# Kernel optimization log

Measured on AMD Instinct MI355X. Metric: run time of the kernel, lower is better.

The kernel has to match this reference:

```python
import jax, jax.numpy as jnp
import numpy as np

NUM_BLOCKS_PER_ROW = 64
NUM_BLOCKS_PER_COLUMN = 36
N = NUM_BLOCKS_PER_ROW * NUM_BLOCKS_PER_COLUMN  # 2304 nodes per frame
F = 32   # frames in the GOP (linear reference chain)
B = 1024  # batch = number of candidate anchor points
S = 256   # selected anchor points


def setup_inputs() -> dict:
    key = jax.random.key(0)
    k1, k2, k3, k4 = jax.random.split(key, 4)
    # weights[f] propagates cumulated error from frame f -> frame f+1; scaled small
    # so the 31-step propagation chain stays numerically tame.
    weights = jax.random.normal(k1, (F - 1, N, N), dtype=jnp.float32) * 0.02
    biases = jax.random.uniform(k2, (F, N), dtype=jnp.float32)  # per-frame tc bias
    selected_anchor_points = jax.random.randint(k3, (S, 3), 0, 32, dtype=jnp.int32)
    candidate_anchor_points = jax.random.randint(k4, (B, 3), 0, 32, dtype=jnp.int32)
    return {
        "weights": weights,
        "biases": biases,
        "selected_anchor_points": selected_anchor_points,
        "candidate_anchor_points": candidate_anchor_points,
    }


def _forward(weights, biases, selected_anchor_points, candidate_anchor_points):
    dtype = biases.dtype
    # flatten (row, col) -> node index, same as row * num_blocks_per_row + col
    sel_f = selected_anchor_points[:, 0]
    sel_node = selected_anchor_points[:, 1] * NUM_BLOCKS_PER_ROW + selected_anchor_points[:, 2]
    cand_f = candidate_anchor_points[:, 0]
    cand_node = candidate_anchor_points[:, 1] * NUM_BLOCKS_PER_ROW + candidate_anchor_points[:, 2]

    # selected anchors zero a node's column for ALL batch rows in their frame
    keep_sel = jnp.ones((F, N), dtype=dtype).at[sel_f, sel_node].set(0.0)  # [F, N]
    # candidate anchors zero one (batch, node) entry in their frame
    cand_oh = jax.nn.one_hot(cand_node, N, dtype=dtype)  # [B, N]

    def apply_masks(err, f):
        # err: [B, N] cumulated error of frame f
        err = err * keep_sel[f][None, :]
        kill = (cand_f == f).astype(dtype)[:, None] * cand_oh  # [B, N]
        return err * (1.0 - kill)

    # root (key) frame: bias only
    err0 = apply_masks(jnp.broadcast_to(biases[0], (B, N)), 0)
    total0 = jnp.sum(err0, axis=1)  # [B]

    def step(carry, xs):
        prev_err, total = carry
        w_f, b_f, f = xs
        # torch.sparse.mm(W, prev.T).T == prev @ W.T
        cur = b_f[None, :] + jnp.matmul(prev_err, w_f.T)  # [B, N]
        cur = apply_masks(cur, f)
        return (cur, total + jnp.sum(cur, axis=1)), None

    frame_ids = jnp.arange(1, F)
    (_, total), _ = jax.lax.scan(step, (err0, total0), (weights, biases[1:], frame_ids))
    return total  # [B] per-candidate summed error


def reference(weights, biases, selected_anchor_points, candidate_anchor_points):
    return _forward(weights, biases, selected_anchor_points, candidate_anchor_points)
```

## Files before the change

kernel.cpp:

```cpp
#include <hip/hip_runtime.h>
#include <stdint.h>

#define NN 2304
#define NF 32
#define NB 1024
#define NS 256

#define BM 128
#define BN 96
#define BK 64
#define KSLICES (NN / BK)
#define DEPTH 4
#define NGRP 8
#define GRPBLKS 24

typedef short bf16x8 __attribute__((ext_vector_type(8)));
typedef float f32x4  __attribute__((ext_vector_type(4)));

__device__ __forceinline__ unsigned short f2bf(float f) {
  union { float f; unsigned u; } v; v.f = f;
  return (unsigned short)((v.u + 0x7FFFu + ((v.u >> 16) & 1u)) >> 16);
}

__device__ __forceinline__ void async16(const void* g, void* l) {
  __builtin_amdgcn_global_load_lds((const __attribute__((address_space(1))) void*)g,
                                   (__attribute__((address_space(3))) void*)l, 16, 0, 0);
}

#define WAITV(n) asm volatile("s_waitcnt vmcnt(" #n ")" ::: "memory")

__global__ void init_kernel(const f32x4* __restrict__ W4, const int* __restrict__ sel,
                            const int* __restrict__ cand, bf16x8* __restrict__ Wb8,
                            float* __restrict__ keep, int* __restrict__ cf,
                            int* __restrict__ cn, float* __restrict__ out,
                            int* __restrict__ bar) {
  int gid = blockIdx.x * 256 + threadIdx.x;
  if (gid < (31 * NN * NN) / 8) {
    f32x4 x = W4[2 * gid], y = W4[2 * gid + 1];
    bf16x8 o;
    o[0] = (short)f2bf(x[0]); o[1] = (short)f2bf(x[1]);
    o[2] = (short)f2bf(x[2]); o[3] = (short)f2bf(x[3]);
    o[4] = (short)f2bf(y[0]); o[5] = (short)f2bf(y[1]);
    o[6] = (short)f2bf(y[2]); o[7] = (short)f2bf(y[3]);
    Wb8[gid] = o;
  }
  if (gid < NF * NN) {
    int f = gid / NN, n = gid - f * NN;
    float v = 1.0f;
    for (int s = 0; s < NS; ++s) {
      int sf = sel[3 * s], sn = sel[3 * s + 1] * 64 + sel[3 * s + 2];
      if (sf == f && sn == n) v = 0.0f;
    }
    keep[gid] = v;
  }
  if (gid < NB) {
    cf[gid] = cand[3 * gid];
    cn[gid] = cand[3 * gid + 1] * 64 + cand[3 * gid + 2];
    out[gid] = 0.f;
  }
  if (gid < NGRP * NF) bar[gid] = 0;
}

__device__ __forceinline__ void group_barrier(int* cnt, int t) {
  __syncthreads();
  if (t == 0) {
    __builtin_amdgcn_fence(__ATOMIC_RELEASE, "agent");
    __hip_atomic_fetch_add(cnt, 1, __ATOMIC_RELAXED, __HIP_MEMORY_SCOPE_AGENT);
    while (__hip_atomic_load(cnt, __ATOMIC_RELAXED, __HIP_MEMORY_SCOPE_AGENT) < GRPBLKS)
      __builtin_amdgcn_s_sleep(2);
    __builtin_amdgcn_fence(__ATOMIC_ACQUIRE, "agent");
  }
  __syncthreads();
}

__launch_bounds__(512, 2)
__global__ void persist_kernel(const unsigned short* __restrict__ Wb,
                               const float* __restrict__ biases,
                               const float* __restrict__ keep,
                               const int* __restrict__ cf, const int* __restrict__ cn,
                               unsigned short* __restrict__ errA,
                               unsigned short* __restrict__ errB,
                               float* __restrict__ out, int* __restrict__ bar) {
  __shared__ __align__(16) unsigned char sA[DEPTH][BM * BK * 2];
  __shared__ __align__(16) unsigned char sB[DEPTH][BN * BK * 2];

  const int t = threadIdx.x;
  const int l = t & 63, w = t >> 6;
  const int wm = w >> 1, wn = w & 1;
  const int id = blockIdx.x;
  const int g = id & 7;
  const int mBase = g * BM;
  const int nBase = (id >> 3) * BN;

  {
    const int row = mBase + (t >> 2);
    const int c0 = nBase + (t & 3) * 24;
    const int kn = (cf[row] == 0) ? cn[row] : -1;
    float sum = 0.f;
    for (int j = 0; j < 24; ++j) {
      const int col = c0 + j;
      float v = biases[col] * keep[col];
      if (col == kn) v = 0.f;
      errA[row * NN + col] = f2bf(v);
      sum += v;
    }
    sum += __shfl_xor(sum, 1, 64);
    sum += __shfl_xor(sum, 2, 64);
    if ((t & 3) == 0) atomicAdd(&out[row], sum);
  }
  group_barrier(&bar[g * NF + 0], t);

  const int sRow = l >> 3;
  const int sCk = (l & 7) ^ sRow;
  const bool aRole = (w < 4);
  const int rw = aRole ? w : (w - 4);
  const int ldsOff = aRole ? (rw * 32 * 128 + l * 16) : (rw * 24 * 128 + l * 16);
  const int gRowOff = aRole ? ((mBase + rw * 32 + sRow) * NN + sCk * 8)
                            : ((nBase + rw * 24 + sRow) * NN + sCk * 8);

  const int fl = l & 15, q = l >> 4;
  const int fragB0 = (q ^ (fl & 7)) * 16;

  for (int f = 1; f < NF; ++f) {
    const unsigned short* Ain = (f & 1) ? errA : errB;
    unsigned short* errOut = (f & 1) ? errB : errA;
    const unsigned short* gSrc =
        (aRole ? Ain : Wb + (size_t)(f - 1) * NN * NN) + gRowOff;
    const float* biasf = biases + f * NN;
    const float* keepf = keep + f * NN;

    f32x4 acc[2][3];
#pragma unroll
    for (int r = 0; r < 2; ++r)
#pragma unroll
      for (int c = 0; c < 3; ++c) acc[r][c] = (f32x4){0.f, 0.f, 0.f, 0.f};

#pragma unroll
    for (int p = 0; p < DEPTH; ++p) {
      const unsigned short* gp = gSrc + p * BK;
      if (aRole) {
        unsigned char* la = &sA[p][ldsOff];
#pragma unroll
        for (int c = 0; c < 4; ++c) async16(gp + c * 8 * NN, la + c * 8 * 128);
      } else {
        unsigned char* lb = &sB[p][ldsOff];
#pragma unroll
        for (int c = 0; c < 3; ++c) async16(gp + c * 8 * NN, lb + c * 8 * 128);
      }
    }

    int buf = 0;
    for (int s = 0; s < KSLICES; ++s) {
      const int ahead = KSLICES - 1 - s;
      if (ahead >= 3) { if (aRole) WAITV(12); else WAITV(9); }
      else if (ahead == 2) { if (aRole) WAITV(8); else WAITV(6); }
      else if (ahead == 1) { if (aRole) WAITV(4); else WAITV(3); }
      else { WAITV(0); }
      asm volatile("s_barrier" ::: "memory");

      const unsigned char* pa = &sA[buf][(wm * 32 + fl) * 128];
      const unsigned char* pb = &sB[buf][(wn * 48 + fl) * 128];
#pragma unroll
      for (int h = 0; h < 2; ++h) {
        const int cb = fragB0 ^ (h * 64);
        bf16x8 aF[2], bF[3];
#pragma unroll
        for (int r = 0; r < 2; ++r) aF[r] = *(const bf16x8*)(pa + r * 2048 + cb);
#pragma unroll
        for (int c = 0; c < 3; ++c) bF[c] = *(const bf16x8*)(pb + c * 2048 + cb);
#pragma unroll
        for (int r = 0; r < 2; ++r)
#pragma unroll
          for (int c = 0; c < 3; ++c)
            acc[r][c] = __builtin_amdgcn_mfma_f32_16x16x32_bf16(aF[r], bF[c], acc[r][c], 0, 0, 0);
      }
      asm volatile("s_waitcnt lgkmcnt(0)\n\ts_barrier" ::: "memory");
      if (s + DEPTH < KSLICES) {
        const unsigned short* gp = gSrc + (s + DEPTH) * BK;
        if (aRole) {
          unsigned char* la = &sA[buf][ldsOff];
#pragma unroll
          for (int c = 0; c < 4; ++c) async16(gp + c * 8 * NN, la + c * 8 * 128);
        } else {
          unsigned char* lb = &sB[buf][ldsOff];
#pragma unroll
          for (int c = 0; c < 3; ++c) async16(gp + c * 8 * NN, lb + c * 8 * 128);
        }
      }
      buf = (buf == DEPTH - 1) ? 0 : buf + 1;
    }

#pragma unroll
    for (int r = 0; r < 2; ++r) {
      float rs[4] = {0.f, 0.f, 0.f, 0.f};
      const int rowB = mBase + wm * 32 + r * 16 + q * 4;
#pragma unroll
      for (int c = 0; c < 3; ++c) {
        const int col = nBase + wn * 48 + c * 16 + fl;
        const float kv = keepf[col], bv = biasf[col];
#pragma unroll
        for (int i = 0; i < 4; ++i) {
          const int row = rowB + i;
          float v = (acc[r][c][i] + bv) * kv;
          if (cf[row] == f && cn[row] == col) v = 0.f;
          errOut[row * NN + col] = f2bf(v);
          rs[i] += v;
        }
      }
#pragma unroll
      for (int m = 1; m < 16; m <<= 1) {
#pragma unroll
        for (int i = 0; i < 4; ++i) rs[i] += __shfl_xor(rs[i], m, 64);
      }
      if (fl == 0) {
#pragma unroll
        for (int i = 0; i < 4; ++i) atomicAdd(&out[rowB + i], rs[i]);
      }
    }

    group_barrier(&bar[g * NF + f], t);
  }
}

extern "C" void kernel_launch(void* const* d_in, const int* in_sizes, int n_in,
                              void* d_out, int out_size, void* d_ws, size_t ws_size,
                              hipStream_t stream) {
  (void)in_sizes; (void)n_in; (void)out_size; (void)ws_size;
  const float* W = (const float*)d_in[0];
  const float* biases = (const float*)d_in[1];
  const int* sel = (const int*)d_in[2];
  const int* cand = (const int*)d_in[3];
  float* out = (float*)d_out;
  char* ws = (char*)d_ws;

  size_t off = 0;
  unsigned short* Wb = (unsigned short*)(ws + off); off += (size_t)31 * NN * NN * 2;
  float* keep = (float*)(ws + off); off += (size_t)NF * NN * 4;
  int* cf = (int*)(ws + off); off += NB * 4;
  int* cn = (int*)(ws + off); off += NB * 4;
  int* bar = (int*)(ws + off); off += NGRP * NF * 4;
  off = (off + 255) & ~(size_t)255;
  unsigned short* errA = (unsigned short*)(ws + off); off += (size_t)NB * NN * 2;
  unsigned short* errB = (unsigned short*)(ws + off);

  int convBlocks = (31 * NN * NN / 8 + 255) / 256;
  init_kernel<<<convBlocks, 256, 0, stream>>>((const f32x4*)W, sel, cand, (bf16x8*)Wb,
                                              keep, cf, cn, out, bar);

  const unsigned short* WbC = Wb;
  void* kargs[] = {(void*)&WbC, (void*)&biases, (void*)&keep, (void*)&cf, (void*)&cn,
                   (void*)&errA, (void*)&errB, (void*)&out, (void*)&bar};
  hipError_t e = hipLaunchCooperativeKernel(
      reinterpret_cast<void*>(persist_kernel), dim3(NGRP * GRPBLKS), dim3(512),
      kargs, 0, stream);
  if (e != hipSuccess) {
    persist_kernel<<<NGRP * GRPBLKS, 512, 0, stream>>>(Wb, biases, keep, cf, cn,
                                                       errA, errB, out, bar);
  }
}
```

Baseline: 1.969 ms.

## Split init kernel, scatter selected masks, and use five-buffer LDS ring

The monolithic init kernel is split into a grid-stride weight conversion, a mask build that fills keep with ones, and a small scatter kernel that zeroes the selected-anchor entries. This replaces the per-element 256-iteration loop over selected anchors. The GEMM main loop now uses five LDS buffers with separate read and write indices, so the next slice's async load is issued right after the barrier. That removes the second barrier and the lgkmcnt wait per slice, and s_setprio raises priority around the MFMA block. The extra buffer increases LDS use per block, which could limit occupancy under the 2-blocks-per-CU launch bound.

```diff
diff --git a/kernel.cpp b/kernel.cpp
--- a/kernel.cpp
+++ b/kernel.cpp
@@ -11,6 +11,7 @@
 #define BK 64
 #define KSLICES (NN / BK)
 #define DEPTH 4
+#define NBUF 5
 #define NGRP 8
 #define GRPBLKS 24
 
@@ -29,13 +30,9 @@
 
 #define WAITV(n) asm volatile("s_waitcnt vmcnt(" #n ")" ::: "memory")
 
-__global__ void init_kernel(const f32x4* __restrict__ W4, const int* __restrict__ sel,
-                            const int* __restrict__ cand, bf16x8* __restrict__ Wb8,
-                            float* __restrict__ keep, int* __restrict__ cf,
-                            int* __restrict__ cn, float* __restrict__ out,
-                            int* __restrict__ bar) {
-  int gid = blockIdx.x * 256 + threadIdx.x;
-  if (gid < (31 * NN * NN) / 8) {
+__global__ void convert_w(const f32x4* __restrict__ W4, bf16x8* __restrict__ Wb8) {
+  const int total = (31 * NN * NN) / 8;
+  for (int gid = blockIdx.x * 256 + threadIdx.x; gid < total; gid += gridDim.x * 256) {
     f32x4 x = W4[2 * gid], y = W4[2 * gid + 1];
     bf16x8 o;
     o[0] = (short)f2bf(x[0]); o[1] = (short)f2bf(x[1]);
@@ -44,21 +41,25 @@
     o[6] = (short)f2bf(y[2]); o[7] = (short)f2bf(y[3]);
     Wb8[gid] = o;
   }
-  if (gid < NF * NN) {
-    int f = gid / NN, n = gid - f * NN;
-    float v = 1.0f;
-    for (int s = 0; s < NS; ++s) {
-      int sf = sel[3 * s], sn = sel[3 * s + 1] * 64 + sel[3 * s + 2];
-      if (sf == f && sn == n) v = 0.0f;
-    }
-    keep[gid] = v;
-  }
+}
+
+__global__ void build_masks(const int* __restrict__ cand, float* __restrict__ keep,
+                            int* __restrict__ cf, int* __restrict__ cn,
+                            float* __restrict__ out, int* __restrict__ bar) {
+  int gid = blockIdx.x * 256 + threadIdx.x;
+  if (gid < NF * NN) keep[gid] = 1.0f;
   if (gid < NB) {
     cf[gid] = cand[3 * gid];
     cn[gid] = cand[3 * gid + 1] * 64 + cand[3 * gid + 2];
     out[gid] = 0.f;
   }
   if (gid < NGRP * NF) bar[gid] = 0;
+}
+
+__global__ void scatter_sel(const int* __restrict__ sel, float* __restrict__ keep) {
+  int s = threadIdx.x;
+  int sf = sel[3 * s], sn = sel[3 * s + 1] * 64 + sel[3 * s + 2];
+  keep[sf * NN + sn] = 0.0f;
 }
 
 __device__ __forceinline__ void group_barrier(int* cnt, int t) {
@@ -81,8 +82,8 @@
                                unsigned short* __restrict__ errA,
                                unsigned short* __restrict__ errB,
                                float* __restrict__ out, int* __restrict__ bar) {
-  __shared__ __align__(16) unsigned char sA[DEPTH][BM * BK * 2];
-  __shared__ __align__(16) unsigned char sB[DEPTH][BN * BK * 2];
+  __shared__ __align__(16) unsigned char sA[NBUF][BM * BK * 2];
+  __shared__ __align__(16) unsigned char sB[NBUF][BN * BK * 2];
 
   const int t = threadIdx.x;
   const int l = t & 63, w = t >> 6;
@@ -149,7 +150,7 @@
       }
     }
 
-    int buf = 0;
+    int rbuf = 0, wbuf = DEPTH;
     for (int s = 0; s < KSLICES; ++s) {
       const int ahead = KSLICES - 1 - s;
       if (ahead >= 3) { if (aRole) WAITV(12); else WAITV(9); }
@@ -157,9 +158,22 @@
       else if (ahead == 1) { if (aRole) WAITV(4); else WAITV(3); }
       else { WAITV(0); }
       asm volatile("s_barrier" ::: "memory");
-
-      const unsigned char* pa = &sA[buf][(wm * 32 + fl) * 128];
-      const unsigned char* pb = &sB[buf][(wn * 48 + fl) * 128];
+      if (s + DEPTH < KSLICES) {
+        const unsigned short* gp = gSrc + (s + DEPTH) * BK;
+        if (aRole) {
+          unsigned char* la = &sA[wbuf][ldsOff];
+#pragma unroll
+          for (int c = 0; c < 4; ++c) async16(gp + c * 8 * NN, la + c * 8 * 128);
+        } else {
+          unsigned char* lb = &sB[wbuf][ldsOff];
+#pragma unroll
+          for (int c = 0; c < 3; ++c) async16(gp + c * 8 * NN, lb + c * 8 * 128);
+        }
+      }
+
+      const unsigned char* pa = &sA[rbuf][(wm * 32 + fl) * 128];
+      const unsigned char* pb = &sB[rbuf][(wn * 48 + fl) * 128];
+      __builtin_amdgcn_s_setprio(1);
 #pragma unroll
       for (int h = 0; h < 2; ++h) {
         const int cb = fragB0 ^ (h * 64);
@@ -174,20 +188,9 @@
           for (int c = 0; c < 3; ++c)
             acc[r][c] = __builtin_amdgcn_mfma_f32_16x16x32_bf16(aF[r], bF[c], acc[r][c], 0, 0, 0);
       }
-      asm volatile("s_waitcnt lgkmcnt(0)\n\ts_barrier" ::: "memory");
-      if (s + DEPTH < KSLICES) {
-        const unsigned short* gp = gSrc + (s + DEPTH) * BK;
-        if (aRole) {
-          unsigned char* la = &sA[buf][ldsOff];
-#pragma unroll
-          for (int c = 0; c < 4; ++c) async16(gp + c * 8 * NN, la + c * 8 * 128);
-        } else {
-          unsigned char* lb = &sB[buf][ldsOff];
-#pragma unroll
-          for (int c = 0; c < 3; ++c) async16(gp + c * 8 * NN, lb + c * 8 * 128);
-        }
-      }
-      buf = (buf == DEPTH - 1) ? 0 : buf + 1;
+      __builtin_amdgcn_s_setprio(0);
+      rbuf = (rbuf == NBUF - 1) ? 0 : rbuf + 1;
+      wbuf = (wbuf == NBUF - 1) ? 0 : wbuf + 1;
     }
 
 #pragma unroll
@@ -243,9 +246,9 @@
   unsigned short* errA = (unsigned short*)(ws + off); off += (size_t)NB * NN * 2;
   unsigned short* errB = (unsigned short*)(ws + off);
 
-  int convBlocks = (31 * NN * NN / 8 + 255) / 256;
-  init_kernel<<<convBlocks, 256, 0, stream>>>((const f32x4*)W, sel, cand, (bf16x8*)Wb,
-                                              keep, cf, cn, out, bar);
+  convert_w<<<4096, 256, 0, stream>>>((const f32x4*)W, (bf16x8*)Wb);
+  build_masks<<<(NF * NN + 255) / 256, 256, 0, stream>>>(cand, keep, cf, cn, out, bar);
+  scatter_sel<<<1, NS, 0, stream>>>(sel, keep);
 
   const unsigned short* WbC = Wb;
   void* kargs[] = {(void*)&WbC, (void*)&biases, (void*)&keep, (void*)&cf, (void*)&cn,
```

New measurement: 1.977 ms. Within noise of the previous version (+0.4%).
